# Kernel tuning notes

Measured on AMD Instinct MI355X. Metric: run time of the kernel, lower is better.

Reference implementation:

```python
import jax, jax.numpy as jnp
import numpy as np
from jax import lax

B_, N_, DIM, HEADS, WS, HW = 16, 3136, 512, 8, 7, 56
SD = DIM // 2          # single_dim per branch (mul=[1,1])
S = SD // HEADS        # per-branch head dim


def setup_inputs() -> dict:
    key = jax.random.key(0)
    ks = jax.random.split(key, 12)
    r = lambda i, shape, sc=0.02: jax.random.normal(ks[i], shape, jnp.float32) * sc
    return dict(
        x=jax.random.normal(ks[0], (B_, N_, DIM), jnp.float32),
        H=HW, W=HW,
        q_w=r(1, (DIM, DIM)),
        kv_dw_w=r(2, (DIM, 1, 3, 3), 0.3), kv_dw_b=jnp.zeros((DIM,), jnp.float32),
        kv_pw_w=r(3, (DIM, DIM, 1, 1), 0.05), kv_pw_b=jnp.zeros((DIM,), jnp.float32),
        fc_w0=r(4, (S, S)), fc_w1=r(5, (S, S)),
        single_w0=r(6, (2 * S, S)), single_w1=r(7, (2 * S, S)),
        local_w0=r(8, (SD, 1, 3, 3), 0.3), local_b0=jnp.zeros((SD,), jnp.float32),
        local_w1=r(9, (SD, 1, 3, 3), 0.3), local_b1=jnp.zeros((SD,), jnp.float32),
        proj_w=r(10, (DIM, DIM)), proj_b=jnp.zeros((DIM,), jnp.float32),
    )


def _dwconv(x, w, b):
    # depthwise 3x3, padding 1 (NCHW / OIHW)
    y = lax.conv_general_dilated(x, w, (1, 1), [(1, 1), (1, 1)],
                                 feature_group_count=x.shape[1],
                                 dimension_numbers=('NCHW', 'OIHW', 'NCHW'))
    return y + b[None, :, None, None]


def _pwconv(x, w, b):
    y = lax.conv_general_dilated(x, w, (1, 1), [(0, 0), (0, 0)],
                                 dimension_numbers=('NCHW', 'OIHW', 'NCHW'))
    return y + b[None, :, None, None]


def _unfold(x, k, stride, dil):
    # nn.Unfold(kernel_size=k, stride=stride, padding=0, dilation=dil): [B,C,H,W] -> [B, C*k*k, L]
    B, C, H, W = x.shape
    L = (H - (dil * (k - 1) + 1)) // stride + 1  # H == W here
    idx = (jnp.arange(L) * stride)[:, None] + jnp.arange(k) * dil  # [L, k]
    t = x[:, :, idx, :]            # [B,C,Lh,kh,W]
    t = t[:, :, :, :, idx]         # [B,C,Lh,kh,Lw,kw]
    t = t.transpose(0, 1, 3, 5, 2, 4)  # [B,C,kh,kw,Lh,Lw] -> torch unfold channel order
    return t.reshape(B, C * k * k, L * L)


def reference(x, H, W, q_w, kv_dw_w, kv_dw_b, kv_pw_w, kv_pw_b,
              fc_w0, fc_w1, single_w0, single_w1,
              local_w0, local_b0, local_w1, local_b1, proj_w, proj_b):
    B, N, C = x.shape
    q = (x @ q_w.T).reshape(B, N, HEADS, C // HEADS).transpose(0, 2, 1, 3)  # [B,h,N,C/h]
    xim = x.reshape(B, H, W, C).transpose(0, 3, 1, 2)
    kv = _pwconv(_dwconv(xim, kv_dw_w, kv_dw_b), kv_pw_w, kv_pw_b)  # [B,C,H,W]
    branches = [(fc_w0, single_w0, local_w0, local_b0),
                (fc_w1, single_w1, local_w1, local_b1)]
    outs = []
    for i, (fc_w, single_w, lw, lb) in enumerate(branches):
        dil = 2 ** i
        stride = dil * (WS - 1) + 1
        q_ = q[:, :, :, i * S:(i + 1) * S]                      # [B,h,N,S]
        u = _unfold(kv[:, i * SD:(i + 1) * SD], WS, stride, dil)  # [B, SD*49, L]
        L = u.shape[-1]
        u = u.reshape(B, HEADS, S, WS * WS, L).transpose(0, 1, 3, 4, 2)  # [B,h,49,L,S]
        u = u.reshape(B, HEADS, WS * WS, L * S)
        # AdaptiveAvgPool2d((None, S)): mean over consecutive chunks of length L
        pooled = u.reshape(B, HEADS, WS * WS, S, L).mean(-1)     # [B,h,49,S]
        kvp = (pooled @ fc_w.T) @ single_w.T                     # [B,h,49,2S]
        k_, v_ = kvp[..., :S], kvp[..., S:]
        attn = jax.nn.softmax((q_ @ k_.transpose(0, 1, 3, 2)) * (S ** -0.5), axis=-1)  # [B,h,N,49]
        vimg = v_.transpose(0, 1, 3, 2).reshape(B, SD, WS, WS)
        v_ = v_ + _dwconv(vimg, lw, lb).reshape(B, HEADS, S, WS * WS).transpose(0, 1, 3, 2)
        outs.append((attn @ v_).transpose(0, 2, 1, 3).reshape(B, N, SD))
    return jnp.concatenate(outs, -1) @ proj_w.T + proj_b
```

## Files before the change

### kernel.cpp

```cpp
#include <hip/hip_runtime.h>


typedef _Float16 __attribute__((ext_vector_type(8))) f16x8;
typedef float __attribute__((ext_vector_type(4))) f32x4;

#define NB    16
#define NTOK  3136
#define CDIM  512
#define HWDIM 56

__device__ __forceinline__ void gll16(const void* g, void* l) {
    __builtin_amdgcn_global_load_lds((const __attribute__((address_space(1))) void*)g,
                                     (__attribute__((address_space(3))) void*)l, 16, 0, 0);
}

__global__ __launch_bounds__(256) void cast_f2h(const float* __restrict__ in,
                                                _Float16* __restrict__ out, int n8) {
    int i = blockIdx.x * 256 + threadIdx.x;
    if (i >= n8) return;
    const float4* p = (const float4*)in + (size_t)i * 2;
    float4 a = p[0], b = p[1];
    f16x8 o;
    o[0] = (_Float16)a.x; o[1] = (_Float16)a.y; o[2] = (_Float16)a.z; o[3] = (_Float16)a.w;
    o[4] = (_Float16)b.x; o[5] = (_Float16)b.y; o[6] = (_Float16)b.z; o[7] = (_Float16)b.w;
    *(f16x8*)(out + (size_t)i * 8) = o;
}

__global__ __launch_bounds__(256) void transpose_w(const float* __restrict__ w,
                                                   float* __restrict__ wt) {
    int i = blockIdx.x * 256 + threadIdx.x;
    if (i >= 512 * 9) return;
    int c = i / 9, t = i - c * 9;
    wt[t * 512 + c] = w[i];
}

__global__ __launch_bounds__(256) void dwconv3x3(const _Float16* __restrict__ xh,
                                                 const float* __restrict__ wt,
                                                 const float* __restrict__ bias,
                                                 _Float16* __restrict__ out) {
    const int pr = blockIdx.x * 4 + (threadIdx.x >> 6);
    const int c0 = (threadIdx.x & 63) * 8;
    const int b  = pr / (28 * HWDIM);
    const int rm = pr - b * (28 * HWDIM);
    const int hp = rm / HWDIM;
    const int w  = rm - hp * HWDIM;
    const int h0 = hp * 2;

    float wr[9][8];
#pragma unroll
    for (int t = 0; t < 9; ++t) {
        float4 a = *(const float4*)(wt + t * 512 + c0);
        float4 d = *(const float4*)(wt + t * 512 + c0 + 4);
        wr[t][0] = a.x; wr[t][1] = a.y; wr[t][2] = a.z; wr[t][3] = a.w;
        wr[t][4] = d.x; wr[t][5] = d.y; wr[t][6] = d.z; wr[t][7] = d.w;
    }
    float acc0[8], acc1[8];
    {
        float4 a = *(const float4*)(bias + c0);
        float4 d = *(const float4*)(bias + c0 + 4);
        acc0[0] = a.x; acc0[1] = a.y; acc0[2] = a.z; acc0[3] = a.w;
        acc0[4] = d.x; acc0[5] = d.y; acc0[6] = d.z; acc0[7] = d.w;
#pragma unroll
        for (int j = 0; j < 8; ++j) acc1[j] = acc0[j];
    }
#pragma unroll
    for (int rr = 0; rr < 4; ++rr) {
        const int row = h0 - 1 + rr;
        if ((unsigned)row >= HWDIM) continue;
#pragma unroll
        for (int kw = 0; kw < 3; ++kw) {
            const int ww = w + kw - 1;
            if ((unsigned)ww >= HWDIM) continue;
            f16x8 v = *(const f16x8*)(xh + ((size_t)(b * NTOK + row * HWDIM + ww) * CDIM + c0));
            if (rr < 3) {
                const int t = rr * 3 + kw;
#pragma unroll
                for (int j = 0; j < 8; ++j) acc0[j] += (float)v[j] * wr[t][j];
            }
            if (rr > 0) {
                const int t = (rr - 1) * 3 + kw;
#pragma unroll
                for (int j = 0; j < 8; ++j) acc1[j] += (float)v[j] * wr[t][j];
            }
        }
    }
    f16x8 o0, o1;
#pragma unroll
    for (int j = 0; j < 8; ++j) { o0[j] = (_Float16)acc0[j]; o1[j] = (_Float16)acc1[j]; }
    const size_t p0 = (size_t)(b * NTOK + h0 * HWDIM + w) * CDIM + c0;
    *(f16x8*)(out + p0) = o0;
    *(f16x8*)(out + p0 + (size_t)HWDIM * CDIM) = o1;
}

template <int MODE>
__global__ __launch_bounds__(256) void gemm_bt(const _Float16* __restrict__ A,
                                               const _Float16* __restrict__ B,
                                               const float* __restrict__ bias,
                                               _Float16* __restrict__ Ch,
                                               float* __restrict__ Cf,
                                               int M, int N, int K) {
    __shared__ _Float16 As[128 * 64];
    __shared__ _Float16 Bs[128 * 64];
    const int tid = threadIdx.x;
    const int lane = tid & 63;
    const int wave = tid >> 6;
    const size_t m0 = (size_t)blockIdx.x * 128;
    const int n0 = blockIdx.y * 128;
    const int wm = wave >> 1, wn = wave & 1;
    const int lr = lane & 15, lk = lane >> 4;
    const int srow = wave * 8 + (lane >> 3);
    const int scol = (lane & 7) * 8;
    f32x4 acc[4][4] = {};
    for (int kt = 0; kt < K; kt += 64) {
#pragma unroll
        for (int j = 0; j < 4; ++j) {
            gll16(A + ((m0 + j * 32 + srow) * K + kt + scol), &As[j * 2048 + wave * 512]);
            gll16(B + ((size_t)(n0 + j * 32 + srow) * K + kt + scol), &Bs[j * 2048 + wave * 512]);
        }
        __syncthreads();
#pragma unroll
        for (int ks = 0; ks < 2; ++ks) {
            f16x8 af[4], bf[4];
#pragma unroll
            for (int mi = 0; mi < 4; ++mi)
                af[mi] = *(const f16x8*)&As[(wm * 64 + mi * 16 + lr) * 64 + ks * 32 + lk * 8];
#pragma unroll
            for (int ni = 0; ni < 4; ++ni)
                bf[ni] = *(const f16x8*)&Bs[(wn * 64 + ni * 16 + lr) * 64 + ks * 32 + lk * 8];
#pragma unroll
            for (int mi = 0; mi < 4; ++mi)
#pragma unroll
                for (int ni = 0; ni < 4; ++ni)
                    acc[mi][ni] = __builtin_amdgcn_mfma_f32_16x16x32_f16(af[mi], bf[ni], acc[mi][ni], 0, 0, 0);
        }
        __syncthreads();
    }
#pragma unroll
    for (int mi = 0; mi < 4; ++mi)
#pragma unroll
        for (int ni = 0; ni < 4; ++ni) {
            const int col = n0 + wn * 64 + ni * 16 + lr;
            float bv = 0.f;
            if constexpr (MODE >= 1) bv = bias[col];
#pragma unroll
            for (int j = 0; j < 4; ++j) {
                const size_t row = m0 + wm * 64 + mi * 16 + lk * 4 + j;
                float v = acc[mi][ni][j] + bv;
                if constexpr (MODE == 2) Cf[row * N + col] = v;
                else Ch[row * N + col] = (_Float16)v;
            }
        }
}

__global__ __launch_bounds__(256) void kv_small(const _Float16* __restrict__ kvh,
                                                const float* __restrict__ fc0, const float* __restrict__ fc1,
                                                const float* __restrict__ sg0, const float* __restrict__ sg1,
                                                const float* __restrict__ lw0, const float* __restrict__ lb0,
                                                const float* __restrict__ lw1, const float* __restrict__ lb1,
                                                _Float16* __restrict__ Kb, _Float16* __restrict__ Vb) {
    const int head = blockIdx.x;
    const int br = blockIdx.y;
    const int b = blockIdx.z;
    const float* fc = br ? fc1 : fc0;
    const float* sg = br ? sg1 : sg0;
    const float* lw = br ? lw1 : lw0;
    const float* lb = br ? lb1 : lb0;
    __shared__ float pooled[49 * 32];
    __shared__ float tmp[49 * 32];
    __shared__ float kvp[49 * 64];
    const int tid = threadIdx.x;
    if (br == 0) {
        for (int idx = tid; idx < 49 * 64; idx += 256) {
            int w = idx >> 6, l = idx & 63;
            int ly = l >> 3, lx = l & 7, pp = w / 7, qq = w % 7;
            int n = (ly * 7 + pp) * HWDIM + (lx * 7 + qq);
            const f16x8* src = (const f16x8*)(kvh + ((size_t)(b * NTOK + n) * CDIM + head * 32));
            float s = 0;
#pragma unroll
            for (int t = 0; t < 4; ++t) {
                f16x8 v = src[t];
#pragma unroll
                for (int j = 0; j < 8; ++j) s += (float)v[j];
            }
            kvp[idx] = s;
        }
        __syncthreads();
        for (int idx = tid; idx < 49 * 32; idx += 256) {
            int w = idx >> 5, sp = idx & 31;
            pooled[idx] = (kvp[(w << 6) + 2 * sp] + kvp[(w << 6) + 2 * sp + 1]) * (1.f / 64.f);
        }
    } else {
        for (int idx = tid; idx < 49 * 32; idx += 256) {
            int w = idx >> 5, t = idx & 31;
            int l = t >> 1, hf = t & 1;
            int ly = l >> 2, lx = l & 3, pp = w / 7, qq = w % 7;
            int n = (ly * 13 + pp * 2) * HWDIM + (lx * 13 + qq * 2);
            const f16x8* src = (const f16x8*)(kvh + ((size_t)(b * NTOK + n) * CDIM + 256 + head * 32 + hf * 16));
            float s = 0;
#pragma unroll
            for (int t2 = 0; t2 < 2; ++t2) {
                f16x8 v = src[t2];
#pragma unroll
                for (int j = 0; j < 8; ++j) s += (float)v[j];
            }
            pooled[idx] = s * (1.f / 16.f);
        }
    }
    __syncthreads();
    for (int idx = tid; idx < 49 * 32; idx += 256) {
        int w = idx >> 5, j = idx & 31;
        float s = 0;
#pragma unroll
        for (int k = 0; k < 32; ++k) s += pooled[(w << 5) + k] * fc[j * 32 + k];
        tmp[idx] = s;
    }
    __syncthreads();
    for (int idx = tid; idx < 49 * 64; idx += 256) {
        int w = idx >> 6, o = idx & 63;
        float s = 0;
#pragma unroll
        for (int k = 0; k < 32; ++k) s += tmp[(w << 5) + k] * sg[o * 32 + k];
        kvp[idx] = s;
    }
    __syncthreads();
    const size_t base = (((size_t)b * 2 + br) * 8 + head) * 1568;
    for (int idx = tid; idx < 49 * 32; idx += 256) {
        int w = idx >> 5, sp = idx & 31;
        Kb[base + idx] = (_Float16)kvp[(w << 6) + sp];
        int pp = w / 7, qq = w % 7;
        int c = head * 32 + sp;
        float a = kvp[(w << 6) + 32 + sp] + lb[c];
#pragma unroll
        for (int kh = 0; kh < 3; ++kh) {
            int p2 = pp + kh - 1;
            if ((unsigned)p2 >= 7) continue;
#pragma unroll
            for (int kw = 0; kw < 3; ++kw) {
                int q2 = qq + kw - 1;
                if ((unsigned)q2 >= 7) continue;
                a += kvp[((p2 * 7 + q2) << 6) + 32 + sp] * lw[c * 9 + kh * 3 + kw];
            }
        }
        Vb[base + idx] = (_Float16)a;
    }
}

__global__ __launch_bounds__(256) void attn_fused(const _Float16* __restrict__ qh,
                                                  const _Float16* __restrict__ Kb,
                                                  const _Float16* __restrict__ Vb,
                                                  _Float16* __restrict__ outh) {
    const int b = blockIdx.y;
    const int br = blockIdx.z >> 3;
    const int head = blockIdx.z & 7;
    __shared__ _Float16 Kp[64 * 40];
    __shared__ _Float16 Vt[32 * 72];
    __shared__ _Float16 Pl[4][64 * 72];
    const int tid = threadIdx.x;
    const int lane = tid & 63, wave = tid >> 6;
    const size_t kvbase = (((size_t)b * 2 + br) * 8 + head) * 1568;
    for (int idx = tid; idx < 64 * 40; idx += 256) {
        int r = idx / 40, c = idx - r * 40;
        Kp[idx] = (r < 49 && c < 32) ? Kb[kvbase + r * 32 + c] : (_Float16)0.f;
    }
    for (int idx = tid; idx < 32 * 72; idx += 256) {
        int s = idx / 72, w = idx - s * 72;
        Vt[idx] = (w < 49) ? Vb[kvbase + w * 32 + s] : (_Float16)0.f;
    }
    __syncthreads();
    const int mtile = blockIdx.x * 4 + wave;
    if (mtile >= 49) return;
    const int n0 = mtile * 64;
    const int lr = lane & 15, lk = lane >> 4;
    f16x8 qf[4], kf[4];
    const size_t qrow0 = ((size_t)b * NTOK + n0) * CDIM + head * 64 + br * 32 + lk * 8;
#pragma unroll
    for (int mi = 0; mi < 4; ++mi)
        qf[mi] = *(const f16x8*)(qh + qrow0 + (size_t)(mi * 16 + lr) * CDIM);
#pragma unroll
    for (int ni = 0; ni < 4; ++ni)
        kf[ni] = *(const f16x8*)&Kp[(ni * 16 + lr) * 40 + lk * 8];
    f32x4 sacc[4][4] = {};
#pragma unroll
    for (int mi = 0; mi < 4; ++mi)
#pragma unroll
        for (int ni = 0; ni < 4; ++ni)
            sacc[mi][ni] = __builtin_amdgcn_mfma_f32_16x16x32_f16(qf[mi], kf[ni], sacc[mi][ni], 0, 0, 0);
    float den[4][4];
#pragma unroll
    for (int mi = 0; mi < 4; ++mi)
#pragma unroll
        for (int j = 0; j < 4; ++j) den[mi][j] = 0.f;
    const float SCALE = 0.17677669529663687f;
#pragma unroll
    for (int mi = 0; mi < 4; ++mi)
#pragma unroll
        for (int ni = 0; ni < 4; ++ni) {
            const bool valid = (ni * 16 + lr) < 49;
#pragma unroll
            for (int j = 0; j < 4; ++j) {
                float e = valid ? __expf(sacc[mi][ni][j] * SCALE) : 0.f;
                sacc[mi][ni][j] = e;
                den[mi][j] += e;
            }
        }
#pragma unroll
    for (int mi = 0; mi < 4; ++mi)
#pragma unroll
        for (int j = 0; j < 4; ++j) {
            float d = den[mi][j];
            d += __shfl_xor(d, 1);
            d += __shfl_xor(d, 2);
            d += __shfl_xor(d, 4);
            d += __shfl_xor(d, 8);
            den[mi][j] = 1.f / d;
        }
    _Float16* P = Pl[wave];
#pragma unroll
    for (int mi = 0; mi < 4; ++mi)
#pragma unroll
        for (int ni = 0; ni < 4; ++ni)
#pragma unroll
            for (int j = 0; j < 4; ++j)
                P[(mi * 16 + lk * 4 + j) * 72 + ni * 16 + lr] =
                    (_Float16)(sacc[mi][ni][j] * den[mi][j]);
    f32x4 oacc[4][2] = {};
#pragma unroll
    for (int k0 = 0; k0 < 2; ++k0) {
        f16x8 vf0 = *(const f16x8*)&Vt[lr * 72 + k0 * 32 + lk * 8];
        f16x8 vf1 = *(const f16x8*)&Vt[(16 + lr) * 72 + k0 * 32 + lk * 8];
#pragma unroll
        for (int mi = 0; mi < 4; ++mi) {
            f16x8 pf = *(const f16x8*)&P[(mi * 16 + lr) * 72 + k0 * 32 + lk * 8];
            oacc[mi][0] = __builtin_amdgcn_mfma_f32_16x16x32_f16(pf, vf0, oacc[mi][0], 0, 0, 0);
            oacc[mi][1] = __builtin_amdgcn_mfma_f32_16x16x32_f16(pf, vf1, oacc[mi][1], 0, 0, 0);
        }
    }
    const size_t obase = ((size_t)b * NTOK + n0) * CDIM + br * 256 + head * 32;
#pragma unroll
    for (int mi = 0; mi < 4; ++mi)
#pragma unroll
        for (int ci = 0; ci < 2; ++ci)
#pragma unroll
            for (int j = 0; j < 4; ++j)
                outh[obase + (size_t)(mi * 16 + lk * 4 + j) * CDIM + ci * 16 + lr] =
                    (_Float16)oacc[mi][ci][j];
}

extern "C" void kernel_launch(void* const* d_in, const int* in_sizes, int n_in,
                              void* d_out, int out_size, void* d_ws, size_t ws_size,
                              hipStream_t stream) {
    const float* x       = (const float*)d_in[0];
    const float* q_w     = (const float*)d_in[3];
    const float* kv_dw_w = (const float*)d_in[4];
    const float* kv_dw_b = (const float*)d_in[5];
    const float* kv_pw_w = (const float*)d_in[6];
    const float* kv_pw_b = (const float*)d_in[7];
    const float* fc_w0   = (const float*)d_in[8];
    const float* fc_w1   = (const float*)d_in[9];
    const float* sg_w0   = (const float*)d_in[10];
    const float* sg_w1   = (const float*)d_in[11];
    const float* lw0     = (const float*)d_in[12];
    const float* lb0     = (const float*)d_in[13];
    const float* lw1     = (const float*)d_in[14];
    const float* lb1     = (const float*)d_in[15];
    const float* proj_w  = (const float*)d_in[16];
    const float* proj_b  = (const float*)d_in[17];

    char* ws = (char*)d_ws;
    const size_t SZ_BIG = (size_t)50176 * 512 * 2;
    _Float16* XH  = (_Float16*)(ws);
    _Float16* KVH = XH;
    _Float16* DW  = (_Float16*)(ws + SZ_BIG);
    _Float16* AO  = DW;
    _Float16* QH  = (_Float16*)(ws + 2 * SZ_BIG);
    _Float16* WQ  = (_Float16*)(ws + 3 * SZ_BIG);
    _Float16* WPW = WQ + 262144;
    _Float16* WPJ = WPW + 262144;
    _Float16* KB  = WPJ + 262144;
    _Float16* VB  = KB + (size_t)16 * 2 * 8 * 49 * 32;
    float*    WT  = (float*)(VB + (size_t)16 * 2 * 8 * 49 * 32);

    cast_f2h<<<dim3(12544), dim3(256), 0, stream>>>(x, XH, 25690112 / 8);
    cast_f2h<<<dim3(128), dim3(256), 0, stream>>>(q_w, WQ, 32768);
    cast_f2h<<<dim3(128), dim3(256), 0, stream>>>(kv_pw_w, WPW, 32768);
    cast_f2h<<<dim3(128), dim3(256), 0, stream>>>(proj_w, WPJ, 32768);
    transpose_w<<<dim3(18), dim3(256), 0, stream>>>(kv_dw_w, WT);

    dwconv3x3<<<dim3(6272), dim3(256), 0, stream>>>(XH, WT, kv_dw_b, DW);

    gemm_bt<0><<<dim3(392, 4), dim3(256), 0, stream>>>(XH, WQ, nullptr, QH, nullptr, 50176, 512, 512);
    gemm_bt<1><<<dim3(392, 4), dim3(256), 0, stream>>>(DW, WPW, kv_pw_b, KVH, nullptr, 50176, 512, 512);

    kv_small<<<dim3(8, 2, 16), dim3(256), 0, stream>>>(KVH, fc_w0, fc_w1, sg_w0, sg_w1,
                                                       lw0, lb0, lw1, lb1, KB, VB);

    attn_fused<<<dim3(13, 16, 16), dim3(256), 0, stream>>>(QH, KB, VB, AO);

    gemm_bt<2><<<dim3(392, 4), dim3(256), 0, stream>>>(AO, WPJ, proj_b, nullptr, (float*)d_out,
                                                       50176, 512, 512);
}
```

Measured before the change: 506.2 us.

## Use head-sliced Q and attention-output layouts, merge weight prep kernels

The Q projection now writes its output in a per-(batch, 32-channel slice) contiguous layout, so each attention head reads a dense block of Q. The attention kernel stages its output through shared memory and writes 16-byte vectors into the same sliced layout. The final projection GEMM gathers its A operand from that layout. The four weight cast/transpose launches are merged into one prep kernel, K is loaded into shared memory with vector loads, and the P buffer is halved by processing 32 rows at a time. The goal is to replace strided 2-byte global stores and strided Q reads with coalesced accesses, at the cost of div/mod index math in the GEMM load and store paths.

```diff
diff --git a/kernel.cpp b/kernel.cpp
--- a/kernel.cpp
+++ b/kernel.cpp
@@ -2,12 +2,14 @@
 
 
 typedef _Float16 __attribute__((ext_vector_type(8))) f16x8;
+typedef _Float16 __attribute__((ext_vector_type(4))) f16x4;
 typedef float __attribute__((ext_vector_type(4))) f32x4;
 
 #define NB    16
 #define NTOK  3136
 #define CDIM  512
 #define HWDIM 56
+#define SLICE 100352
 
 __device__ __forceinline__ void gll16(const void* g, void* l) {
     __builtin_amdgcn_global_load_lds((const __attribute__((address_space(1))) void*)g,
@@ -26,12 +28,32 @@
     *(f16x8*)(out + (size_t)i * 8) = o;
 }
 
-__global__ __launch_bounds__(256) void transpose_w(const float* __restrict__ w,
-                                                   float* __restrict__ wt) {
-    int i = blockIdx.x * 256 + threadIdx.x;
-    if (i >= 512 * 9) return;
-    int c = i / 9, t = i - c * 9;
-    wt[t * 512 + c] = w[i];
+__global__ __launch_bounds__(256) void prep(const float* __restrict__ q_w,
+                                            const float* __restrict__ pw_w,
+                                            const float* __restrict__ pj_w,
+                                            const float* __restrict__ dw_w,
+                                            _Float16* __restrict__ WQ,
+                                            _Float16* __restrict__ WPW,
+                                            _Float16* __restrict__ WPJ,
+                                            float* __restrict__ WT) {
+    int bid = blockIdx.x;
+    if (bid < 384) {
+        const float* src = bid < 128 ? q_w : (bid < 256 ? pw_w : pj_w);
+        _Float16* dst = bid < 128 ? WQ : (bid < 256 ? WPW : WPJ);
+        int i = (bid & 127) * 256 + threadIdx.x;
+        const float4* p = (const float4*)src + (size_t)i * 2;
+        float4 a = p[0], b = p[1];
+        f16x8 o;
+        o[0] = (_Float16)a.x; o[1] = (_Float16)a.y; o[2] = (_Float16)a.z; o[3] = (_Float16)a.w;
+        o[4] = (_Float16)b.x; o[5] = (_Float16)b.y; o[6] = (_Float16)b.z; o[7] = (_Float16)b.w;
+        *(f16x8*)(dst + (size_t)i * 8) = o;
+    } else {
+        int i = (bid - 384) * 256 + threadIdx.x;
+        if (i < 512 * 9) {
+            int c = i / 9, t = i - c * 9;
+            WT[t * 512 + c] = dw_w[i];
+        }
+    }
 }
 
 __global__ __launch_bounds__(256) void dwconv3x3(const _Float16* __restrict__ xh,
@@ -110,12 +132,37 @@
     const int lr = lane & 15, lk = lane >> 4;
     const int srow = wave * 8 + (lane >> 3);
     const int scol = (lane & 7) * 8;
+
+    unsigned bj[4], nj[4];
+    const int shalf = scol >> 5;
+    const int wcol = scol & 31;
+    if constexpr (MODE == 2) {
+#pragma unroll
+        for (int j = 0; j < 4; ++j) {
+            unsigned row = (unsigned)m0 + j * 32 + srow;
+            bj[j] = row / 3136u;
+            nj[j] = row - bj[j] * 3136u;
+        }
+    }
+
     f32x4 acc[4][4] = {};
     for (int kt = 0; kt < K; kt += 64) {
-#pragma unroll
-        for (int j = 0; j < 4; ++j) {
-            gll16(A + ((m0 + j * 32 + srow) * K + kt + scol), &As[j * 2048 + wave * 512]);
-            gll16(B + ((size_t)(n0 + j * 32 + srow) * K + kt + scol), &Bs[j * 2048 + wave * 512]);
+        if constexpr (MODE == 2) {
+            const int s = (kt >> 5) + shalf;
+            const size_t soff = (size_t)s * SLICE + wcol;
+#pragma unroll
+            for (int j = 0; j < 4; ++j) {
+                gll16(A + (size_t)bj[j] * 16 * SLICE + soff + (size_t)nj[j] * 32,
+                      &As[j * 2048 + wave * 512]);
+                gll16(B + ((size_t)(n0 + j * 32 + srow) * K + kt + scol),
+                      &Bs[j * 2048 + wave * 512]);
+            }
+        } else {
+#pragma unroll
+            for (int j = 0; j < 4; ++j) {
+                gll16(A + ((m0 + j * 32 + srow) * K + kt + scol), &As[j * 2048 + wave * 512]);
+                gll16(B + ((size_t)(n0 + j * 32 + srow) * K + kt + scol), &Bs[j * 2048 + wave * 512]);
+            }
         }
         __syncthreads();
 #pragma unroll
@@ -135,21 +182,38 @@
         }
         __syncthreads();
     }
-#pragma unroll
-    for (int mi = 0; mi < 4; ++mi)
-#pragma unroll
-        for (int ni = 0; ni < 4; ++ni) {
-            const int col = n0 + wn * 64 + ni * 16 + lr;
-            float bv = 0.f;
-            if constexpr (MODE >= 1) bv = bias[col];
-#pragma unroll
-            for (int j = 0; j < 4; ++j) {
-                const size_t row = m0 + wm * 64 + mi * 16 + lk * 4 + j;
-                float v = acc[mi][ni][j] + bv;
-                if constexpr (MODE == 2) Cf[row * N + col] = v;
-                else Ch[row * N + col] = (_Float16)v;
-            }
-        }
+
+    if constexpr (MODE == 0) {
+#pragma unroll
+        for (int mi = 0; mi < 4; ++mi)
+#pragma unroll
+            for (int ni = 0; ni < 4; ++ni) {
+                const int col = n0 + wn * 64 + ni * 16 + lr;
+                const int sl = col >> 5, sc = col & 31;
+#pragma unroll
+                for (int j = 0; j < 4; ++j) {
+                    unsigned row = (unsigned)m0 + wm * 64 + mi * 16 + lk * 4 + j;
+                    unsigned bb = row / 3136u, nn = row - bb * 3136u;
+                    Ch[((size_t)bb * 16 + sl) * SLICE + (size_t)nn * 32 + sc] =
+                        (_Float16)acc[mi][ni][j];
+                }
+            }
+    } else {
+#pragma unroll
+        for (int mi = 0; mi < 4; ++mi)
+#pragma unroll
+            for (int ni = 0; ni < 4; ++ni) {
+                const int col = n0 + wn * 64 + ni * 16 + lr;
+                const float bv = bias[col];
+#pragma unroll
+                for (int j = 0; j < 4; ++j) {
+                    const size_t row = m0 + wm * 64 + mi * 16 + lk * 4 + j;
+                    float v = acc[mi][ni][j] + bv;
+                    if constexpr (MODE == 2) Cf[row * N + col] = v;
+                    else Ch[row * N + col] = (_Float16)v;
+                }
+            }
+    }
 }
 
 __global__ __launch_bounds__(256) void kv_small(const _Float16* __restrict__ kvh,
@@ -245,37 +309,41 @@
     }
 }
 
-__global__ __launch_bounds__(256) void attn_fused(const _Float16* __restrict__ qh,
+__global__ __launch_bounds__(256) void attn_fused(const _Float16* __restrict__ Qp,
                                                   const _Float16* __restrict__ Kb,
                                                   const _Float16* __restrict__ Vb,
-                                                  _Float16* __restrict__ outh) {
+                                                  _Float16* __restrict__ AOp) {
     const int b = blockIdx.y;
     const int br = blockIdx.z >> 3;
     const int head = blockIdx.z & 7;
     __shared__ _Float16 Kp[64 * 40];
     __shared__ _Float16 Vt[32 * 72];
-    __shared__ _Float16 Pl[4][64 * 72];
+    __shared__ _Float16 Pw[4][32 * 72];
     const int tid = threadIdx.x;
     const int lane = tid & 63, wave = tid >> 6;
     const size_t kvbase = (((size_t)b * 2 + br) * 8 + head) * 1568;
-    for (int idx = tid; idx < 64 * 40; idx += 256) {
-        int r = idx / 40, c = idx - r * 40;
-        Kp[idx] = (r < 49 && c < 32) ? Kb[kvbase + r * 32 + c] : (_Float16)0.f;
-    }
-    for (int idx = tid; idx < 32 * 72; idx += 256) {
-        int s = idx / 72, w = idx - s * 72;
-        Vt[idx] = (w < 49) ? Vb[kvbase + w * 32 + s] : (_Float16)0.f;
+    {
+        int r = tid >> 2, ck = tid & 3;
+        f16x8 v = {};
+        if (r < 49) v = *(const f16x8*)(Kb + kvbase + r * 32 + ck * 8);
+        *(f16x8*)&Kp[r * 40 + ck * 8] = v;
+    }
+    for (int idx = tid; idx < 64 * 32; idx += 256) {
+        int w = idx >> 5, s = idx & 31;
+        Vt[s * 72 + w] = (w < 49) ? Vb[kvbase + w * 32 + s] : (_Float16)0.f;
     }
     __syncthreads();
     const int mtile = blockIdx.x * 4 + wave;
     if (mtile >= 49) return;
     const int n0 = mtile * 64;
     const int lr = lane & 15, lk = lane >> 4;
+    const size_t qsl = ((size_t)b * 16 + head * 2 + br) * SLICE + (size_t)n0 * 32;
+    const size_t osl = ((size_t)b * 16 + br * 8 + head) * SLICE + (size_t)n0 * 32;
+
     f16x8 qf[4], kf[4];
-    const size_t qrow0 = ((size_t)b * NTOK + n0) * CDIM + head * 64 + br * 32 + lk * 8;
-#pragma unroll
-    for (int mi = 0; mi < 4; ++mi)
-        qf[mi] = *(const f16x8*)(qh + qrow0 + (size_t)(mi * 16 + lr) * CDIM);
+#pragma unroll
+    for (int mi = 0; mi < 4; ++mi)
+        qf[mi] = *(const f16x8*)(Qp + qsl + (size_t)(mi * 16 + lr) * 32 + lk * 8);
 #pragma unroll
     for (int ni = 0; ni < 4; ++ni)
         kf[ni] = *(const f16x8*)&Kp[(ni * 16 + lr) * 40 + lk * 8];
@@ -285,6 +353,7 @@
 #pragma unroll
         for (int ni = 0; ni < 4; ++ni)
             sacc[mi][ni] = __builtin_amdgcn_mfma_f32_16x16x32_f16(qf[mi], kf[ni], sacc[mi][ni], 0, 0, 0);
+
     float den[4][4];
 #pragma unroll
     for (int mi = 0; mi < 4; ++mi)
@@ -314,36 +383,54 @@
             d += __shfl_xor(d, 8);
             den[mi][j] = 1.f / d;
         }
-    _Float16* P = Pl[wave];
+    f16x4 ph[4][4];
 #pragma unroll
     for (int mi = 0; mi < 4; ++mi)
 #pragma unroll
         for (int ni = 0; ni < 4; ++ni)
 #pragma unroll
             for (int j = 0; j < 4; ++j)
-                P[(mi * 16 + lk * 4 + j) * 72 + ni * 16 + lr] =
-                    (_Float16)(sacc[mi][ni][j] * den[mi][j]);
-    f32x4 oacc[4][2] = {};
-#pragma unroll
-    for (int k0 = 0; k0 < 2; ++k0) {
-        f16x8 vf0 = *(const f16x8*)&Vt[lr * 72 + k0 * 32 + lk * 8];
-        f16x8 vf1 = *(const f16x8*)&Vt[(16 + lr) * 72 + k0 * 32 + lk * 8];
-#pragma unroll
-        for (int mi = 0; mi < 4; ++mi) {
-            f16x8 pf = *(const f16x8*)&P[(mi * 16 + lr) * 72 + k0 * 32 + lk * 8];
-            oacc[mi][0] = __builtin_amdgcn_mfma_f32_16x16x32_f16(pf, vf0, oacc[mi][0], 0, 0, 0);
-            oacc[mi][1] = __builtin_amdgcn_mfma_f32_16x16x32_f16(pf, vf1, oacc[mi][1], 0, 0, 0);
-        }
-    }
-    const size_t obase = ((size_t)b * NTOK + n0) * CDIM + br * 256 + head * 32;
-#pragma unroll
-    for (int mi = 0; mi < 4; ++mi)
-#pragma unroll
-        for (int ci = 0; ci < 2; ++ci)
-#pragma unroll
-            for (int j = 0; j < 4; ++j)
-                outh[obase + (size_t)(mi * 16 + lk * 4 + j) * CDIM + ci * 16 + lr] =
-                    (_Float16)oacc[mi][ci][j];
+                ph[mi][ni][j] = (_Float16)(sacc[mi][ni][j] * den[mi][j]);
+
+    _Float16* P = Pw[wave];
+#pragma unroll
+    for (int h = 0; h < 2; ++h) {
+#pragma unroll
+        for (int mh = 0; mh < 2; ++mh) {
+            const int mi = h * 2 + mh;
+#pragma unroll
+            for (int ni = 0; ni < 4; ++ni)
+#pragma unroll
+                for (int j = 0; j < 4; ++j)
+                    P[(mh * 16 + lk * 4 + j) * 72 + ni * 16 + lr] = ph[mi][ni][j];
+        }
+        f32x4 oacc[2][2] = {};
+#pragma unroll
+        for (int k0 = 0; k0 < 2; ++k0) {
+            f16x8 vf0 = *(const f16x8*)&Vt[lr * 72 + k0 * 32 + lk * 8];
+            f16x8 vf1 = *(const f16x8*)&Vt[(16 + lr) * 72 + k0 * 32 + lk * 8];
+#pragma unroll
+            for (int mh = 0; mh < 2; ++mh) {
+                f16x8 pf = *(const f16x8*)&P[(mh * 16 + lr) * 72 + k0 * 32 + lk * 8];
+                oacc[mh][0] = __builtin_amdgcn_mfma_f32_16x16x32_f16(pf, vf0, oacc[mh][0], 0, 0, 0);
+                oacc[mh][1] = __builtin_amdgcn_mfma_f32_16x16x32_f16(pf, vf1, oacc[mh][1], 0, 0, 0);
+            }
+        }
+#pragma unroll
+        for (int mh = 0; mh < 2; ++mh)
+#pragma unroll
+            for (int ci = 0; ci < 2; ++ci)
+#pragma unroll
+                for (int j = 0; j < 4; ++j)
+                    P[(mh * 16 + lk * 4 + j) * 40 + ci * 16 + lr] = (_Float16)(oacc[mh][ci][j]);
+#pragma unroll
+        for (int t = 0; t < 2; ++t) {
+            const int idx = t * 64 + lane;
+            const int row = idx >> 2, ck = idx & 3;
+            f16x8 ov = *(const f16x8*)&P[row * 40 + ck * 8];
+            *(f16x8*)(AOp + osl + (size_t)(h * 32 + row) * 32 + ck * 8) = ov;
+        }
+    }
 }
 
 extern "C" void kernel_launch(void* const* d_in, const int* in_sizes, int n_in,
@@ -381,10 +468,7 @@
     float*    WT  = (float*)(VB + (size_t)16 * 2 * 8 * 49 * 32);
 
     cast_f2h<<<dim3(12544), dim3(256), 0, stream>>>(x, XH, 25690112 / 8);
-    cast_f2h<<<dim3(128), dim3(256), 0, stream>>>(q_w, WQ, 32768);
-    cast_f2h<<<dim3(128), dim3(256), 0, stream>>>(kv_pw_w, WPW, 32768);
-    cast_f2h<<<dim3(128), dim3(256), 0, stream>>>(proj_w, WPJ, 32768);
-    transpose_w<<<dim3(18), dim3(256), 0, stream>>>(kv_dw_w, WT);
+    prep<<<dim3(402), dim3(256), 0, stream>>>(q_w, kv_pw_w, proj_w, kv_dw_w, WQ, WPW, WPJ, WT);
 
     dwconv3x3<<<dim3(6272), dim3(256), 0, stream>>>(XH, WT, kv_dw_b, DW);
 
```

New measurement: 486.1 us. 4.0% less time.
